# Optimization experiments

Hardware: AMD Instinct MI355X
Metric: run time of the kernel (lower is better)

## Reference

```python
import jax, jax.numpy as jnp
import numpy as np

B, T, D, H = 2, 2048, 1024, 16
HD = D // H  # head dim = 64; rope half-dim = 32


def setup_inputs() -> dict:
    key = jax.random.key(0)
    ks = jax.random.split(key, 8)
    x = jax.random.normal(ks[0], (B, T, D), dtype=jnp.float32)
    # additive causal mask (upper triangle = -inf-like), as typically passed in
    mask = jnp.triu(jnp.full((T, T), -1e9, dtype=jnp.float32), k=1)
    # standard RoPE angles: theta = pos / 10000^(2i/hd)
    inv_freq = 1.0 / (10000.0 ** (np.arange(0, HD, 2, dtype=np.float32) / HD))
    ang = np.arange(T, dtype=np.float32)[:, None] * inv_freq[None, :]  # [T, HD//2]
    cos = jnp.asarray(np.cos(ang), dtype=jnp.float32)
    sin = jnp.asarray(np.sin(ang), dtype=jnp.float32)
    s = 1.0 / np.sqrt(D)
    Wq = jax.random.normal(ks[1], (D, D), dtype=jnp.float32) * s
    bq = jnp.zeros((D,), dtype=jnp.float32)
    Wk = jax.random.normal(ks[2], (D, D), dtype=jnp.float32) * s
    Wv = jax.random.normal(ks[3], (D, D), dtype=jnp.float32) * s
    bv = jnp.zeros((D,), dtype=jnp.float32)
    Wo = jax.random.normal(ks[4], (D, D), dtype=jnp.float32) * s
    bo = jnp.zeros((D,), dtype=jnp.float32)
    return {"x": x, "mask": mask, "cos": cos, "sin": sin, "Wq": Wq, "bq": bq,
            "Wk": Wk, "Wv": Wv, "bv": bv, "Wo": Wo, "bo": bo}


def _apply_rope(t, cos, sin):
    # t: [B, T, H, HD]; cos/sin: [T, HD//2]; complex multiply on (even, odd) pairs
    t = t.reshape(B, T, H, HD // 2, 2)
    t0, t1 = t[..., 0], t[..., 1]
    c = cos[None, :, None, :]
    s = sin[None, :, None, :]
    out = jnp.stack([t0 * c - t1 * s, t0 * s + t1 * c], axis=-1)
    return out.reshape(B, T, H, HD)


def reference(x, mask, cos, sin, Wq, bq, Wk, Wv, bv, Wo, bo):
    scale = float(HD) ** (-0.25)
    q = (x @ Wq.T + bq).reshape(B, T, H, HD)
    k = (x @ Wk.T).reshape(B, T, H, HD)  # key proj has no bias
    v = (x @ Wv.T + bv).reshape(B, T, H, HD)
    q = _apply_rope(q, cos, sin)
    k = _apply_rope(k, cos, sin)
    q = q.transpose(0, 2, 1, 3) * scale  # [B,H,T,HD]
    k = k.transpose(0, 2, 1, 3) * scale
    v = v.transpose(0, 2, 1, 3)
    qk = jnp.einsum("bhtd,bhsd->bhts", q, k) + mask  # [B,H,T,T]
    qk = qk.astype(jnp.float32)
    w = jax.nn.softmax(qk, axis=-1).astype(q.dtype)
    wv = jnp.einsum("bhts,bhsd->bhtd", w, v)
    wv = wv.transpose(0, 2, 1, 3).reshape(B, T, D)
    out = wv @ Wo.T + bo
    return out, qk
```

## Files before the change

kernel.cpp:

```cpp
#include <hip/hip_runtime.h>
#include <math.h>

#define Tc 2048
#define Dc 1024
#define Hc 16
#define HDc 64
#define BT 4096
#define SCALE 0.35355339059327379f

typedef _Float16 f16;
typedef __attribute__((ext_vector_type(4))) _Float16 f16x4;
typedef __attribute__((ext_vector_type(8))) _Float16 f16x8;
typedef __attribute__((ext_vector_type(4))) float f32x4;

__device__ __forceinline__ void gload16(const f16* g, f16* l)
{
    __builtin_amdgcn_global_load_lds(
        (const __attribute__((address_space(1))) void*)g,
        (__attribute__((address_space(3))) void*)l, 16, 0, 0);
}

__global__ __launch_bounds__(256)
void cast_kernel(const float* __restrict__ x,
                 const float* __restrict__ Wq, const float* __restrict__ Wk,
                 const float* __restrict__ Wv, const float* __restrict__ Wo,
                 f16* __restrict__ xh,
                 f16* __restrict__ Wqh, f16* __restrict__ Wkh,
                 f16* __restrict__ Wvh, f16* __restrict__ Woh)
{
    const int u = blockIdx.y;
    const float* s; f16* d;
    if (u < 4) { s = x + (size_t)u * (1u << 20); d = xh + (size_t)u * (1u << 20); }
    else switch (u) {
        case 4:  s = Wq; d = Wqh; break;
        case 5:  s = Wk; d = Wkh; break;
        case 6:  s = Wv; d = Wvh; break;
        default: s = Wo; d = Woh; break;
    }
    int i = blockIdx.x * 256 + threadIdx.x;
    float4 v = ((const float4*)s)[i];
    f16x4 o = {(f16)v.x, (f16)v.y, (f16)v.z, (f16)v.w};
    ((f16x4*)d)[i] = o;
}

#define GEMM_BODY(Aptr, Bptr)                                                        \
    __shared__ f16 As[128][64];                                                      \
    __shared__ f16 Bs[128][64];                                                      \
    const int tid = threadIdx.x;                                                     \
    const int w = tid >> 6, l = tid & 63;                                            \
    const int lr = l & 15, lq = l >> 4;                                              \
    const int wr = w >> 1, wc = w & 1;                                               \
    const int m0 = blockIdx.y * 128, n0 = blockIdx.x * 128;                          \
    const int srow8 = l >> 3, sslot = l & 7;                                         \
    f32x4 acc[4][4] = {};                                                            \
    for (int k0 = 0; k0 < Dc; k0 += 64) {                                            \
        __syncthreads();                                                             \
        _Pragma("unroll")                                                            \
        for (int c = 0; c < 4; c++) {                                                \
            int chunk = w * 4 + c;                                                   \
            int row = chunk * 8 + srow8;                                             \
            int col = (sslot ^ (row & 7)) * 8;                                       \
            gload16(&Aptr[(size_t)(m0 + row) * Dc + k0 + col],                       \
                    (f16*)((char*)&As[0][0] + chunk * 1024));                        \
            gload16(&Bptr[(size_t)(n0 + row) * Dc + k0 + col],                       \
                    (f16*)((char*)&Bs[0][0] + chunk * 1024));                        \
        }                                                                            \
        __syncthreads();                                                             \
        _Pragma("unroll")                                                            \
        for (int kk = 0; kk < 2; kk++) {                                             \
            f16x8 af[4], bf[4];                                                      \
            _Pragma("unroll")                                                        \
            for (int mi = 0; mi < 4; mi++) {                                         \
                int row = 64 * wr + 16 * mi + lr;                                    \
                int bo = (lq * 16 + kk * 64) ^ ((row & 7) << 4);                     \
                af[mi] = *(const f16x8*)((const char*)&As[0][0] + row * 128 + bo);   \
            }                                                                        \
            _Pragma("unroll")                                                        \
            for (int ni = 0; ni < 4; ni++) {                                         \
                int row = 64 * wc + 16 * ni + lr;                                    \
                int bo = (lq * 16 + kk * 64) ^ ((row & 7) << 4);                     \
                bf[ni] = *(const f16x8*)((const char*)&Bs[0][0] + row * 128 + bo);   \
            }                                                                        \
            _Pragma("unroll")                                                        \
            for (int mi = 0; mi < 4; mi++)                                           \
                _Pragma("unroll")                                                    \
                for (int ni = 0; ni < 4; ni++)                                       \
                    acc[mi][ni] = __builtin_amdgcn_mfma_f32_16x16x32_f16(            \
                        af[mi], bf[ni], acc[mi][ni], 0, 0, 0);                       \
        }                                                                            \
    }

__global__ __launch_bounds__(256)
void qkv_proj_kernel(const f16* __restrict__ xh,
                     const f16* __restrict__ Wqh, const f16* __restrict__ Wkh,
                     const f16* __restrict__ Wvh,
                     const float* __restrict__ bq, const float* __restrict__ bv,
                     f16* __restrict__ qh, f16* __restrict__ kh, f16* __restrict__ vh,
                     const float* __restrict__ cosp, const float* __restrict__ sinp)
{
    const int mode = blockIdx.z;
    const f16* W = (mode == 0) ? Wqh : (mode == 1 ? Wkh : Wvh);
    const float* bias = (mode == 0) ? bq : (mode == 2 ? bv : nullptr);
    f16* dst = (mode == 0) ? qh : (mode == 1 ? kh : vh);

    GEMM_BODY(xh, W)

    #pragma unroll
    for (int mi = 0; mi < 4; mi++) {
        #pragma unroll
        for (int ni = 0; ni < 4; ni++) {
            #pragma unroll
            for (int i = 0; i < 4; i++) {
                int gm = m0 + 64 * wr + 16 * mi + lq * 4 + i;
                int gn = n0 + 64 * wc + 16 * ni + lr;
                float v = acc[mi][ni][i];
                if (bias) v += bias[gn];
                int b = gm >> 11, t = gm & 2047;
                int h = gn >> 6, d = gn & 63;
                if (mode != 2) {
                    float pv = __shfl_xor(v, 1, 64);
                    int p = d >> 1;
                    float c = cosp[t * 32 + p], s = sinp[t * 32 + p];
                    v = (d & 1) ? (pv * s + v * c) : (v * c - pv * s);
                    v *= SCALE;
                }
                dst[((size_t)(b * Hc + h) * Tc + t) * HDc + d] = (f16)v;
            }
        }
    }
}

__global__ __launch_bounds__(256)
void out_proj_kernel(const f16* __restrict__ A, const f16* __restrict__ W,
                     const float* __restrict__ bias, float* __restrict__ out)
{
    GEMM_BODY(A, W)

    #pragma unroll
    for (int mi = 0; mi < 4; mi++)
        #pragma unroll
        for (int ni = 0; ni < 4; ni++)
            #pragma unroll
            for (int i = 0; i < 4; i++) {
                int gm = m0 + 64 * wr + 16 * mi + lq * 4 + i;
                int gn = n0 + 64 * wc + 16 * ni + lr;
                out[(size_t)gm * Dc + gn] = acc[mi][ni][i] + bias[gn];
            }
}

__global__ __launch_bounds__(256)
void flash_kernel(const f16* __restrict__ qh, const f16* __restrict__ kh,
                  const f16* __restrict__ vh, f16* __restrict__ wvh,
                  float* __restrict__ qk)
{
    const int z = blockIdx.y;
    const int t0 = (gridDim.x - 1 - blockIdx.x) * 64;
    const int tid = threadIdx.x;
    const int w = tid >> 6, l = tid & 63;
    const int lr = l & 15, lq = l >> 4;

    __shared__ f16 Qs[64][72];
    __shared__ f16 Ks[64][72];
    __shared__ f16 VsT[64][72];
    __shared__ f16 Ps[64][72];

    const f16* Qg = qh + (size_t)z * Tc * HDc;
    const f16* Kg = kh + (size_t)z * Tc * HDc;
    const f16* Vg = vh + (size_t)z * Tc * HDc;
    float* C = qk + (size_t)z * Tc * Tc;

    {
        int r = tid >> 2, c = (tid & 3) * 16;
        *(f16x8*)&Qs[r][c]     = *(const f16x8*)&Qg[(size_t)(t0 + r) * HDc + c];
        *(f16x8*)&Qs[r][c + 8] = *(const f16x8*)&Qg[(size_t)(t0 + r) * HDc + c + 8];
    }

    {
        int r = t0 + (tid >> 2);
        int n4 = (Tc - t0 - 64) >> 2;
        float4 mv; mv.x = mv.y = mv.z = mv.w = -1e9f;
        float4* rowp = (float4*)(C + (size_t)r * Tc + t0 + 64);
        for (int c = (tid & 3); c < n4; c += 4) rowp[c] = mv;
    }

    const int kr = tid >> 2, kc = (tid & 3) * 16;
    const int vs = tid & 63, vd = (tid >> 6) * 16;
    f16x8 rk0 = *(const f16x8*)&Kg[(size_t)kr * HDc + kc];
    f16x8 rk1 = *(const f16x8*)&Kg[(size_t)kr * HDc + kc + 8];
    f16x8 rv0 = *(const f16x8*)&Vg[(size_t)vs * HDc + vd];
    f16x8 rv1 = *(const f16x8*)&Vg[(size_t)vs * HDc + vd + 8];

    f32x4 O[4] = {};
    float mrow[4], lrow[4];
    #pragma unroll
    for (int i = 0; i < 4; i++) { mrow[i] = -1e30f; lrow[i] = 0.f; }

    for (int s0 = 0; s0 <= t0; s0 += 64) {
        asm volatile("" ::: "memory");
        __builtin_amdgcn_s_barrier();
        asm volatile("" ::: "memory");

        *(f16x8*)&Ks[kr][kc]     = rk0;
        *(f16x8*)&Ks[kr][kc + 8] = rk1;
        #pragma unroll
        for (int j = 0; j < 8; j++) {
            VsT[vd + j][vs]     = rv0[j];
            VsT[vd + 8 + j][vs] = rv1[j];
        }

        if (s0 + 64 <= t0) {
            const f16* kp = &Kg[(size_t)(s0 + 64 + kr) * HDc + kc];
            const f16* vp = &Vg[(size_t)(s0 + 64 + vs) * HDc + vd];
            rk0 = *(const f16x8*)kp;
            rk1 = *(const f16x8*)(kp + 8);
            rv0 = *(const f16x8*)vp;
            rv1 = *(const f16x8*)(vp + 8);
        }

        asm volatile("s_waitcnt lgkmcnt(0)" ::: "memory");
        __builtin_amdgcn_s_barrier();
        asm volatile("" ::: "memory");

        f32x4 S[4] = {};
        #pragma unroll
        for (int ks = 0; ks < 2; ks++) {
            f16x8 aq = *(const f16x8*)&Qs[16 * w + lr][lq * 8 + 32 * ks];
            #pragma unroll
            for (int ni = 0; ni < 4; ni++) {
                f16x8 bk = *(const f16x8*)&Ks[16 * ni + lr][lq * 8 + 32 * ks];
                S[ni] = __builtin_amdgcn_mfma_f32_16x16x32_f16(aq, bk, S[ni], 0, 0, 0);
            }
        }

        if (s0 == t0) {
            #pragma unroll
            for (int ni = 0; ni < 4; ni++)
                #pragma unroll
                for (int i = 0; i < 4; i++) {
                    int tg = t0 + 16 * w + lq * 4 + i;
                    int sg = s0 + 16 * ni + lr;
                    if (sg > tg) S[ni][i] = -1e9f;
                }
        }

        #pragma unroll
        for (int ni = 0; ni < 4; ni++)
            #pragma unroll
            for (int i = 0; i < 4; i++) {
                int tg = t0 + 16 * w + lq * 4 + i;
                int sg = s0 + 16 * ni + lr;
                C[(size_t)tg * Tc + sg] = S[ni][i];
            }

        #pragma unroll
        for (int i = 0; i < 4; i++) {
            float v = fmaxf(fmaxf(S[0][i], S[1][i]), fmaxf(S[2][i], S[3][i]));
            v = fmaxf(v, __shfl_xor(v, 1, 64));
            v = fmaxf(v, __shfl_xor(v, 2, 64));
            v = fmaxf(v, __shfl_xor(v, 4, 64));
            v = fmaxf(v, __shfl_xor(v, 8, 64));
            float mnew = fmaxf(mrow[i], v);
            float alpha = __expf(mrow[i] - mnew);
            mrow[i] = mnew;
            float rs = 0.f;
            #pragma unroll
            for (int ni = 0; ni < 4; ni++) {
                float p = __expf(S[ni][i] - mnew);
                S[ni][i] = p;
                rs += p;
            }
            rs += __shfl_xor(rs, 1, 64);
            rs += __shfl_xor(rs, 2, 64);
            rs += __shfl_xor(rs, 4, 64);
            rs += __shfl_xor(rs, 8, 64);
            lrow[i] = lrow[i] * alpha + rs;
            #pragma unroll
            for (int ni = 0; ni < 4; ni++) O[ni][i] *= alpha;
        }

        #pragma unroll
        for (int ni = 0; ni < 4; ni++)
            #pragma unroll
            for (int i = 0; i < 4; i++)
                Ps[16 * w + lq * 4 + i][16 * ni + lr] = (f16)S[ni][i];

        #pragma unroll
        for (int ks = 0; ks < 2; ks++) {
            f16x8 ap = *(const f16x8*)&Ps[16 * w + lr][lq * 8 + 32 * ks];
            #pragma unroll
            for (int ni = 0; ni < 4; ni++) {
                f16x8 bv = *(const f16x8*)&VsT[16 * ni + lr][lq * 8 + 32 * ks];
                O[ni] = __builtin_amdgcn_mfma_f32_16x16x32_f16(ap, bv, O[ni], 0, 0, 0);
            }
        }
    }

    const int b = z >> 4, h = z & 15;
    #pragma unroll
    for (int ni = 0; ni < 4; ni++)
        #pragma unroll
        for (int i = 0; i < 4; i++) {
            int tg = t0 + 16 * w + lq * 4 + i;
            int d = 16 * ni + lr;
            float o = O[ni][i] / lrow[i];
            wvh[((size_t)(b * Tc + tg)) * Dc + h * HDc + d] = (f16)o;
        }
}

extern "C" void kernel_launch(void* const* d_in, const int* in_sizes, int n_in,
                              void* d_out, int out_size, void* d_ws, size_t ws_size,
                              hipStream_t stream)
{
    const float* x    = (const float*)d_in[0];
    const float* cosp = (const float*)d_in[2];
    const float* sinp = (const float*)d_in[3];
    const float* Wq   = (const float*)d_in[4];
    const float* bq   = (const float*)d_in[5];
    const float* Wk   = (const float*)d_in[6];
    const float* Wv   = (const float*)d_in[7];
    const float* bv   = (const float*)d_in[8];
    const float* Wo   = (const float*)d_in[9];
    const float* bo   = (const float*)d_in[10];

    float* out = (float*)d_out;
    float* qk  = out + (size_t)BT * Dc;

    f16* ws  = (f16*)d_ws;
    f16* xh  = ws;
    f16* Wqh = xh  + (size_t)BT * Dc;
    f16* Wkh = Wqh + (size_t)Dc * Dc;
    f16* Wvh = Wkh + (size_t)Dc * Dc;
    f16* Woh = Wvh + (size_t)Dc * Dc;
    f16* qh  = Woh + (size_t)Dc * Dc;
    f16* kh  = qh  + (size_t)BT * Dc;
    f16* vh  = kh  + (size_t)BT * Dc;
    f16* wvh = vh  + (size_t)BT * Dc;

    dim3 blk(256);

    cast_kernel<<<dim3(1024, 8), blk, 0, stream>>>(
        x, Wq, Wk, Wv, Wo, xh, Wqh, Wkh, Wvh, Woh);

    qkv_proj_kernel<<<dim3(Dc / 128, BT / 128, 3), blk, 0, stream>>>(
        xh, Wqh, Wkh, Wvh, bq, bv, qh, kh, vh, cosp, sinp);

    flash_kernel<<<dim3(Tc / 64, 32), blk, 0, stream>>>(qh, kh, vh, wvh, qk);

    out_proj_kernel<<<dim3(Dc / 128, BT / 128), blk, 0, stream>>>(wvh, Woh, bo, out);
}
```

Measured before the change: 771.9 us.

## Enlarge flash attention query tile to 128 rows and use nontemporal qk stores

Each flash block now processes 128 query rows (two 16-row MFMA subtiles per wave) instead of 64. Every K/V tile loaded into LDS is therefore reused across twice as many queries, which halves the K/V global traffic and the number of barriers per query. The stores of the large fp32 qk matrix and its masked fill now use nontemporal stores to avoid polluting the cache. In exchange there are half as many blocks (512), more registers per thread, and extra wasted diagonal work, since the causal mask now applies to the last two key tiles.

```diff
diff --git a/kernel.cpp b/kernel.cpp
--- a/kernel.cpp
+++ b/kernel.cpp
@@ -154,15 +154,15 @@
                   float* __restrict__ qk)
 {
     const int z = blockIdx.y;
-    const int t0 = (gridDim.x - 1 - blockIdx.x) * 64;
+    const int t0 = (gridDim.x - 1 - blockIdx.x) * 128;
     const int tid = threadIdx.x;
     const int w = tid >> 6, l = tid & 63;
     const int lr = l & 15, lq = l >> 4;
 
-    __shared__ f16 Qs[64][72];
+    __shared__ f16 Qs[128][72];
     __shared__ f16 Ks[64][72];
     __shared__ f16 VsT[64][72];
-    __shared__ f16 Ps[64][72];
+    __shared__ f16 Ps[128][72];
 
     const f16* Qg = qh + (size_t)z * Tc * HDc;
     const f16* Kg = kh + (size_t)z * Tc * HDc;
@@ -170,17 +170,21 @@
     float* C = qk + (size_t)z * Tc * Tc;
 
     {
-        int r = tid >> 2, c = (tid & 3) * 16;
-        *(f16x8*)&Qs[r][c]     = *(const f16x8*)&Qg[(size_t)(t0 + r) * HDc + c];
-        *(f16x8*)&Qs[r][c + 8] = *(const f16x8*)&Qg[(size_t)(t0 + r) * HDc + c + 8];
+        int r = tid >> 1, c = (tid & 1) * 32;
+        const f16* qp = &Qg[(size_t)(t0 + r) * HDc + c];
+        *(f16x8*)&Qs[r][c]      = *(const f16x8*)qp;
+        *(f16x8*)&Qs[r][c + 8]  = *(const f16x8*)(qp + 8);
+        *(f16x8*)&Qs[r][c + 16] = *(const f16x8*)(qp + 16);
+        *(f16x8*)&Qs[r][c + 24] = *(const f16x8*)(qp + 24);
     }
 
     {
-        int r = t0 + (tid >> 2);
-        int n4 = (Tc - t0 - 64) >> 2;
-        float4 mv; mv.x = mv.y = mv.z = mv.w = -1e9f;
-        float4* rowp = (float4*)(C + (size_t)r * Tc + t0 + 64);
-        for (int c = (tid & 3); c < n4; c += 4) rowp[c] = mv;
+        int r = t0 + (tid >> 1);
+        int n4 = (Tc - t0 - 128) >> 2;
+        f32x4 mv = {-1e9f, -1e9f, -1e9f, -1e9f};
+        f32x4* rowp = (f32x4*)(C + (size_t)r * Tc + t0 + 128);
+        for (int c = (tid & 1); c < n4; c += 2)
+            __builtin_nontemporal_store(mv, rowp + c);
     }
 
     const int kr = tid >> 2, kc = (tid & 3) * 16;
@@ -190,12 +194,15 @@
     f16x8 rv0 = *(const f16x8*)&Vg[(size_t)vs * HDc + vd];
     f16x8 rv1 = *(const f16x8*)&Vg[(size_t)vs * HDc + vd + 8];
 
-    f32x4 O[4] = {};
-    float mrow[4], lrow[4];
+    f32x4 O[2][4] = {};
+    float mrow[2][4], lrow[2][4];
     #pragma unroll
-    for (int i = 0; i < 4; i++) { mrow[i] = -1e30f; lrow[i] = 0.f; }
-
-    for (int s0 = 0; s0 <= t0; s0 += 64) {
+    for (int mi = 0; mi < 2; mi++)
+        #pragma unroll
+        for (int i = 0; i < 4; i++) { mrow[mi][i] = -1e30f; lrow[mi][i] = 0.f; }
+
+    const int send = t0 + 64;
+    for (int s0 = 0; s0 <= send; s0 += 64) {
         asm volatile("" ::: "memory");
         __builtin_amdgcn_s_barrier();
         asm volatile("" ::: "memory");
@@ -208,7 +215,7 @@
             VsT[vd + 8 + j][vs] = rv1[j];
         }
 
-        if (s0 + 64 <= t0) {
+        if (s0 + 64 <= send) {
             const f16* kp = &Kg[(size_t)(s0 + 64 + kr) * HDc + kc];
             const f16* vp = &Vg[(size_t)(s0 + 64 + vs) * HDc + vd];
             rk0 = *(const f16x8*)kp;
@@ -221,90 +228,111 @@
         __builtin_amdgcn_s_barrier();
         asm volatile("" ::: "memory");
 
-        f32x4 S[4] = {};
+        f32x4 S[2][4] = {};
         #pragma unroll
         for (int ks = 0; ks < 2; ks++) {
-            f16x8 aq = *(const f16x8*)&Qs[16 * w + lr][lq * 8 + 32 * ks];
+            f16x8 aq[2];
+            #pragma unroll
+            for (int mi = 0; mi < 2; mi++)
+                aq[mi] = *(const f16x8*)&Qs[32 * w + 16 * mi + lr][lq * 8 + 32 * ks];
             #pragma unroll
             for (int ni = 0; ni < 4; ni++) {
                 f16x8 bk = *(const f16x8*)&Ks[16 * ni + lr][lq * 8 + 32 * ks];
-                S[ni] = __builtin_amdgcn_mfma_f32_16x16x32_f16(aq, bk, S[ni], 0, 0, 0);
-            }
-        }
-
-        if (s0 == t0) {
+                #pragma unroll
+                for (int mi = 0; mi < 2; mi++)
+                    S[mi][ni] = __builtin_amdgcn_mfma_f32_16x16x32_f16(aq[mi], bk, S[mi][ni], 0, 0, 0);
+            }
+        }
+
+        if (s0 + 63 > t0 + 32 * w) {
+            #pragma unroll
+            for (int mi = 0; mi < 2; mi++)
+                #pragma unroll
+                for (int ni = 0; ni < 4; ni++)
+                    #pragma unroll
+                    for (int i = 0; i < 4; i++) {
+                        int tg = t0 + 32 * w + 16 * mi + lq * 4 + i;
+                        int sg = s0 + 16 * ni + lr;
+                        if (sg > tg) S[mi][ni][i] = -1e9f;
+                    }
+        }
+
+        #pragma unroll
+        for (int mi = 0; mi < 2; mi++)
             #pragma unroll
             for (int ni = 0; ni < 4; ni++)
                 #pragma unroll
                 for (int i = 0; i < 4; i++) {
-                    int tg = t0 + 16 * w + lq * 4 + i;
+                    int tg = t0 + 32 * w + 16 * mi + lq * 4 + i;
                     int sg = s0 + 16 * ni + lr;
-                    if (sg > tg) S[ni][i] = -1e9f;
+                    __builtin_nontemporal_store(S[mi][ni][i], &C[(size_t)tg * Tc + sg]);
                 }
-        }
-
-        #pragma unroll
-        for (int ni = 0; ni < 4; ni++)
+
+        #pragma unroll
+        for (int mi = 0; mi < 2; mi++)
             #pragma unroll
             for (int i = 0; i < 4; i++) {
-                int tg = t0 + 16 * w + lq * 4 + i;
-                int sg = s0 + 16 * ni + lr;
-                C[(size_t)tg * Tc + sg] = S[ni][i];
-            }
-
-        #pragma unroll
-        for (int i = 0; i < 4; i++) {
-            float v = fmaxf(fmaxf(S[0][i], S[1][i]), fmaxf(S[2][i], S[3][i]));
-            v = fmaxf(v, __shfl_xor(v, 1, 64));
-            v = fmaxf(v, __shfl_xor(v, 2, 64));
-            v = fmaxf(v, __shfl_xor(v, 4, 64));
-            v = fmaxf(v, __shfl_xor(v, 8, 64));
-            float mnew = fmaxf(mrow[i], v);
-            float alpha = __expf(mrow[i] - mnew);
-            mrow[i] = mnew;
-            float rs = 0.f;
-            #pragma unroll
-            for (int ni = 0; ni < 4; ni++) {
-                float p = __expf(S[ni][i] - mnew);
-                S[ni][i] = p;
-                rs += p;
-            }
-            rs += __shfl_xor(rs, 1, 64);
-            rs += __shfl_xor(rs, 2, 64);
-            rs += __shfl_xor(rs, 4, 64);
-            rs += __shfl_xor(rs, 8, 64);
-            lrow[i] = lrow[i] * alpha + rs;
-            #pragma unroll
-            for (int ni = 0; ni < 4; ni++) O[ni][i] *= alpha;
-        }
-
-        #pragma unroll
-        for (int ni = 0; ni < 4; ni++)
-            #pragma unroll
-            for (int i = 0; i < 4; i++)
-                Ps[16 * w + lq * 4 + i][16 * ni + lr] = (f16)S[ni][i];
+                float v = fmaxf(fmaxf(S[mi][0][i], S[mi][1][i]),
+                                fmaxf(S[mi][2][i], S[mi][3][i]));
+                v = fmaxf(v, __shfl_xor(v, 1, 64));
+                v = fmaxf(v, __shfl_xor(v, 2, 64));
+                v = fmaxf(v, __shfl_xor(v, 4, 64));
+                v = fmaxf(v, __shfl_xor(v, 8, 64));
+                float mnew = fmaxf(mrow[mi][i], v);
+                float alpha = __expf(mrow[mi][i] - mnew);
+                mrow[mi][i] = mnew;
+                float rs = 0.f;
+                #pragma unroll
+                for (int ni = 0; ni < 4; ni++) {
+                    float p = __expf(S[mi][ni][i] - mnew);
+                    S[mi][ni][i] = p;
+                    rs += p;
+                }
+                rs += __shfl_xor(rs, 1, 64);
+                rs += __shfl_xor(rs, 2, 64);
+                rs += __shfl_xor(rs, 4, 64);
+                rs += __shfl_xor(rs, 8, 64);
+                lrow[mi][i] = lrow[mi][i] * alpha + rs;
+                #pragma unroll
+                for (int ni = 0; ni < 4; ni++) O[mi][ni][i] *= alpha;
+            }
+
+        #pragma unroll
+        for (int mi = 0; mi < 2; mi++)
+            #pragma unroll
+            for (int ni = 0; ni < 4; ni++)
+                #pragma unroll
+                for (int i = 0; i < 4; i++)
+                    Ps[32 * w + 16 * mi + lq * 4 + i][16 * ni + lr] = (f16)S[mi][ni][i];
 
         #pragma unroll
         for (int ks = 0; ks < 2; ks++) {
-            f16x8 ap = *(const f16x8*)&Ps[16 * w + lr][lq * 8 + 32 * ks];
+            f16x8 ap[2];
+            #pragma unroll
+            for (int mi = 0; mi < 2; mi++)
+                ap[mi] = *(const f16x8*)&Ps[32 * w + 16 * mi + lr][lq * 8 + 32 * ks];
             #pragma unroll
             for (int ni = 0; ni < 4; ni++) {
                 f16x8 bv = *(const f16x8*)&VsT[16 * ni + lr][lq * 8 + 32 * ks];
-                O[ni] = __builtin_amdgcn_mfma_f32_16x16x32_f16(ap, bv, O[ni], 0, 0, 0);
+                #pragma unroll
+                for (int mi = 0; mi < 2; mi++)
+                    O[mi][ni] = __builtin_amdgcn_mfma_f32_16x16x32_f16(ap[mi], bv, O[mi][ni], 0, 0, 0);
             }
         }
     }
 
     const int b = z >> 4, h = z & 15;
     #pragma unroll
-    for (int ni = 0; ni < 4; ni++)
-        #pragma unroll
-        for (int i = 0; i < 4; i++) {
-            int tg = t0 + 16 * w + lq * 4 + i;
-            int d = 16 * ni + lr;
-            float o = O[ni][i] / lrow[i];
-            wvh[((size_t)(b * Tc + tg)) * Dc + h * HDc + d] = (f16)o;
-        }
+    for (int mi = 0; mi < 2; mi++)
+        #pragma unroll
+        for (int ni = 0; ni < 4; ni++)
+            #pragma unroll
+            for (int i = 0; i < 4; i++) {
+                int tg = t0 + 32 * w + 16 * mi + lq * 4 + i;
+                int d = 16 * ni + lr;
+                float o = O[mi][ni][i] / lrow[mi][i];
+                wvh[((size_t)(b * Tc + tg)) * Dc + h * HDc + d] = (f16)o;
+            }
 }
 
 extern "C" void kernel_launch(void* const* d_in, const int* in_sizes, int n_in,
@@ -344,7 +372,7 @@
     qkv_proj_kernel<<<dim3(Dc / 128, BT / 128, 3), blk, 0, stream>>>(
         xh, Wqh, Wkh, Wvh, bq, bv, qh, kh, vh, cosp, sinp);
 
-    flash_kernel<<<dim3(Tc / 64, 32), blk, 0, stream>>>(qh, kh, vh, wvh, qk);
+    flash_kernel<<<dim3(Tc / 128, 32), blk, 0, stream>>>(qh, kh, vh, wvh, qk);
 
     out_proj_kernel<<<dim3(Dc / 128, BT / 128), blk, 0, stream>>>(wvh, Woh, bo, out);
 }
```

After: 1.139 ms. 1.47x slower.
